# Kernel optimization log

Measured on AMD Instinct MI355X. Metric: run time of the kernel, lower is better.

Reference implementation:

```python
import jax, jax.numpy as jnp
from jax import lax
import numpy as np

D_MODEL = 1024
D_STATE = 16
D_CONV = 4
EXPAND = 2
D_INNER = EXPAND * D_MODEL          # 2048
DT_RANK = D_MODEL // 16             # 64 (mamba 'auto' dt_rank)
B, L = 1, 1024


def setup_inputs() -> dict:
    key = jax.random.key(0)
    ks = jax.random.split(key, 8)

    def nrm(k, shape, s=0.02):
        return jax.random.normal(k, shape, jnp.float32) * s

    def mamba_params(kbase):
        k = jax.random.split(kbase, 7)
        return {
            'in_w': nrm(k[0], (2 * D_INNER, D_MODEL)),            # in_proj (no bias)
            'conv_w': nrm(k[1], (D_INNER, 1, D_CONV), 0.1),       # depthwise causal conv
            'conv_b': nrm(k[2], (D_INNER,), 0.1),
            'xproj_w': nrm(k[3], (DT_RANK + 2 * D_STATE, D_INNER)),
            'dt_w': nrm(k[4], (D_INNER, DT_RANK), 0.1),
            'dt_b': nrm(k[5], (D_INNER,), 0.1),
            'Alog': jnp.log(jnp.broadcast_to(jnp.arange(1., D_STATE + 1, dtype=jnp.float32), (D_INNER, D_STATE))),
            'Dp': jnp.ones((D_INNER,), jnp.float32),
            'out_w': nrm(k[6], (D_MODEL, D_INNER)),
        }

    fw = mamba_params(ks[0])
    bw = mamba_params(ks[1])
    inp = {'x': jax.random.normal(ks[2], (B, L, D_MODEL), jnp.float32)}
    for n, p in fw.items():
        inp['fw_' + n] = p
    for n, p in bw.items():
        inp['bw_' + n] = p
    inp['proj_w'] = nrm(ks[3], (D_MODEL, 2 * D_MODEL))
    inp['proj_b'] = jnp.zeros((D_MODEL,), jnp.float32)
    inp['ln_w'] = jnp.ones((D_MODEL,), jnp.float32)
    inp['ln_b'] = jnp.zeros((D_MODEL,), jnp.float32)
    return inp


def _mamba(x, in_w, conv_w, conv_b, xproj_w, dt_w, dt_b, Alog, Dp, out_w):
    # x: [B, L, d_model]
    xz = x @ in_w.T                                    # [B, L, 2*d_inner]
    xi, z = jnp.split(xz, 2, axis=-1)
    # causal depthwise conv over time
    xc = lax.conv_general_dilated(jnp.swapaxes(xi, 1, 2), conv_w, (1,),
                                  [(D_CONV - 1, 0)], feature_group_count=D_INNER)
    u = jnp.swapaxes(jax.nn.silu(xc + conv_b[None, :, None]), 1, 2)   # [B, L, d_inner]
    x_dbl = u @ xproj_w.T                              # [B, L, dt_rank + 2*d_state]
    dt = x_dbl[..., :DT_RANK]
    Bm = x_dbl[..., DT_RANK:DT_RANK + D_STATE]
    Cm = x_dbl[..., DT_RANK + D_STATE:]
    delta = jax.nn.softplus(dt @ dt_w.T + dt_b)        # [B, L, d_inner]
    A = -jnp.exp(Alog)                                 # [d_inner, d_state]
    dA = jnp.exp(jnp.einsum('bld,dn->bldn', delta, A))
    dBu = jnp.einsum('bld,bln,bld->bldn', delta, Bm, u)

    def step(h, inputs):
        a, b, c = inputs                               # a,b: [B,D,N]; c: [B,N]
        h = a * h + b
        return h, jnp.einsum('bdn,bn->bd', h, c)

    h0 = jnp.zeros((x.shape[0], D_INNER, D_STATE), x.dtype)
    _, ys = lax.scan(step, h0, (jnp.moveaxis(dA, 1, 0), jnp.moveaxis(dBu, 1, 0), jnp.moveaxis(Cm, 1, 0)))
    y = jnp.moveaxis(ys, 0, 1) + u * Dp                # [B, L, d_inner]
    return (y * jax.nn.silu(z)) @ out_w.T              # [B, L, d_model]


def _block(x,
           fw_in_w, fw_conv_w, fw_conv_b, fw_xproj_w, fw_dt_w, fw_dt_b, fw_Alog, fw_Dp, fw_out_w,
           bw_in_w, bw_conv_w, bw_conv_b, bw_xproj_w, bw_dt_w, bw_dt_b, bw_Alog, bw_Dp, bw_out_w,
           proj_w, proj_b, ln_w, ln_b):
    out_fw = _mamba(x, fw_in_w, fw_conv_w, fw_conv_b, fw_xproj_w, fw_dt_w, fw_dt_b, fw_Alog, fw_Dp, fw_out_w) + x
    xb = jnp.flip(x, axis=1)
    out_bw = jnp.flip(_mamba(xb, bw_in_w, bw_conv_w, bw_conv_b, bw_xproj_w, bw_dt_w, bw_dt_b, bw_Alog, bw_Dp, bw_out_w) + xb, axis=1)
    out = jnp.concatenate([out_fw, out_bw], axis=-1) @ proj_w.T + proj_b
    mu = out.mean(-1, keepdims=True)
    var = out.var(-1, keepdims=True)
    return (out - mu) / jnp.sqrt(var + 1e-5) * ln_w + ln_b


def reference(x,
              fw_in_w, fw_conv_w, fw_conv_b, fw_xproj_w, fw_dt_w, fw_dt_b, fw_Alog, fw_Dp, fw_out_w,
              bw_in_w, bw_conv_w, bw_conv_b, bw_xproj_w, bw_dt_w, bw_dt_b, bw_Alog, bw_Dp, bw_out_w,
              proj_w, proj_b, ln_w, ln_b):
    return _block(x,
                  fw_in_w, fw_conv_w, fw_conv_b, fw_xproj_w, fw_dt_w, fw_dt_b, fw_Alog, fw_Dp, fw_out_w,
                  bw_in_w, bw_conv_w, bw_conv_b, bw_xproj_w, bw_dt_w, bw_dt_b, bw_Alog, bw_Dp, bw_out_w,
                  proj_w, proj_b, ln_w, ln_b)
```

## Files before the change

### kernel.cpp

```cpp
#include <hip/hip_runtime.h>

typedef __bf16 bf16;
typedef __bf16 bf16x8 __attribute__((ext_vector_type(8)));
typedef float  f32x4  __attribute__((ext_vector_type(4)));

#define L_SEQ 1024
#define DM    1024
#define DI    2048
#define DTR   64
#define DSTATE 16
#define XD    96
#define NC    32
#define CS    32

__device__ __forceinline__ float bf2f(bf16 v){ return (float)v; }
__device__ __forceinline__ bf16  f2bf(float v){ return (bf16)v; }

__device__ __forceinline__ void gl_lds16(const bf16* g, bf16* l) {
  __builtin_amdgcn_global_load_lds(
      (const __attribute__((address_space(1))) unsigned int*)g,
      (__attribute__((address_space(3))) unsigned int*)l, 16, 0, 0);
}

#define OFF_X      0L
#define OFF_INW    1048576L
#define OFF_XPROJ  9437184L
#define OFF_DTW    9830400L
#define OFF_OUTW   10092544L
#define OFF_PROJW  14286848L
#define CVT_TOTAL  16384000L

__global__ __launch_bounds__(256) void cvt_k(
    const float* __restrict__ x,
    const float* __restrict__ inw0, const float* __restrict__ inw1,
    const float* __restrict__ xp0,  const float* __restrict__ xp1,
    const float* __restrict__ dt0,  const float* __restrict__ dt1,
    const float* __restrict__ ow0,  const float* __restrict__ ow1,
    const float* __restrict__ pw,   bf16* __restrict__ wb)
{
  long i = ((long)blockIdx.x * 256 + threadIdx.x) * 8;
  if (i >= CVT_TOTAL) return;
  const float* src; long off;
  if      (i < OFF_INW)                 { src = x;    off = i - OFF_X; }
  else if (i < OFF_INW + 4194304L)      { src = inw0; off = i - OFF_INW; }
  else if (i < OFF_XPROJ)               { src = inw1; off = i - (OFF_INW + 4194304L); }
  else if (i < OFF_XPROJ + 196608L)     { src = xp0;  off = i - OFF_XPROJ; }
  else if (i < OFF_DTW)                 { src = xp1;  off = i - (OFF_XPROJ + 196608L); }
  else if (i < OFF_DTW + 131072L)       { src = dt0;  off = i - OFF_DTW; }
  else if (i < OFF_OUTW)                { src = dt1;  off = i - (OFF_DTW + 131072L); }
  else if (i < OFF_OUTW + 2097152L)     { src = ow0;  off = i - OFF_OUTW; }
  else if (i < OFF_PROJW)               { src = ow1;  off = i - (OFF_OUTW + 2097152L); }
  else                                  { src = pw;   off = i - OFF_PROJW; }
  f32x4 v0 = *(const f32x4*)(src + off);
  f32x4 v1 = *(const f32x4*)(src + off + 4);
  bf16x8 t;
  #pragma unroll
  for (int q = 0; q < 4; q++) { t[q] = (bf16)v0[q]; t[4+q] = (bf16)v1[q]; }
  *(bf16x8*)(wb + i) = t;
}

template<int BM, int BN>
__global__ __launch_bounds__(256) void gemm_bt(
    const bf16* __restrict__ A, const bf16* __restrict__ B0, const bf16* __restrict__ B1,
    void* __restrict__ Cv,
    int M, int N, int K, int lda, int ldb, int ldc,
    long aOffZ, long cOffZ,
    const float* __restrict__ bias0, const float* __restrict__ bias1,
    int flipA1, int writeBf16, int act,
    const float* __restrict__ xF, int fuseRes)
{
  constexpr int WM = BM / 2, WN = BN / 2;
  constexpr int MI = WM / 16, NJ = WN / 16;
  constexpr int ACALLS = BM / 32;
  constexpr int BCALLS = BN / 32;

  const int tid  = threadIdx.x;
  const int z    = blockIdx.z;
  const bf16*  Bp   = z ? B1 : B0;
  const float* bias = z ? bias1 : bias0;
  const int flip = z ? flipA1 : 0;
  const int bm = blockIdx.x * BM;
  const int bn = blockIdx.y * BN;

  __shared__ bf16 As[BM * 64];
  __shared__ bf16 Bs[BN * 64];

  f32x4 acc[MI][NJ];
  #pragma unroll
  for (int i=0;i<MI;i++)
    #pragma unroll
    for (int j=0;j<NJ;j++) { acc[i][j][0]=0.f; acc[i][j][1]=0.f; acc[i][j][2]=0.f; acc[i][j][3]=0.f; }

  const int wave = tid >> 6;
  const int lane = tid & 63;
  const int wm = (wave >> 1) * WM;
  const int wn = (wave & 1) * WN;
  const int fr  = lane & 15;
  const int frx = fr & 7;
  const int kqc = lane >> 4;

  const bf16* aSrc[ACALLS];
  int aOff[ACALLS];
  #pragma unroll
  for (int t = 0; t < ACALLS; t++) {
    int s = (wave * ACALLS + t) * 64 + lane;
    int r = s >> 3;
    int j = (s & 7) ^ (r & 7);
    int ar = bm + r;
    int agr = flip ? (M - 1 - ar) : ar;
    aSrc[t] = A + (long)z * aOffZ + (long)agr * lda + j * 8;
    aOff[t] = (wave * ACALLS + t) * 512;
  }
  const bf16* bSrc[BCALLS];
  int bOff[BCALLS];
  #pragma unroll
  for (int t = 0; t < BCALLS; t++) {
    int s = (wave * BCALLS + t) * 64 + lane;
    int r = s >> 3;
    int j = (s & 7) ^ (r & 7);
    int br = bn + r; if (br > N - 1) br = N - 1;
    bSrc[t] = Bp + (long)br * ldb + j * 8;
    bOff[t] = (wave * BCALLS + t) * 512;
  }

  for (int k0 = 0; k0 < K; k0 += 64) {
    #pragma unroll
    for (int t = 0; t < ACALLS; t++) gl_lds16(aSrc[t] + k0, &As[aOff[t]]);
    #pragma unroll
    for (int t = 0; t < BCALLS; t++) gl_lds16(bSrc[t] + k0, &Bs[bOff[t]]);
    __syncthreads();

    #pragma unroll
    for (int ks8 = 0; ks8 < 8; ks8 += 4) {
      bf16x8 af[MI], bfr[NJ];
      #pragma unroll
      for (int i=0;i<MI;i++) {
        int row = wm + i*16 + fr;
        af[i]  = *(const bf16x8*)&As[(row * 8 + ((ks8 + kqc) ^ frx)) * 8];
      }
      #pragma unroll
      for (int j=0;j<NJ;j++) {
        int row = wn + j*16 + fr;
        bfr[j] = *(const bf16x8*)&Bs[(row * 8 + ((ks8 + kqc) ^ frx)) * 8];
      }
      #pragma unroll
      for (int i=0;i<MI;i++)
        #pragma unroll
        for (int j=0;j<NJ;j++)
          acc[i][j] = __builtin_amdgcn_mfma_f32_16x16x32_bf16(af[i], bfr[j], acc[i][j], 0, 0, 0);
    }
    __syncthreads();
  }

  const int rr = (lane >> 4) * 4;
  const int cc = lane & 15;
  #pragma unroll
  for (int i=0;i<MI;i++) {
    #pragma unroll
    for (int j=0;j<NJ;j++) {
      int gn = bn + wn + j*16 + cc;
      if (gn >= N) continue;
      float bv = bias ? bias[gn] : 0.f;
      #pragma unroll
      for (int r=0;r<4;r++) {
        int gm = bm + wm + i*16 + rr + r;
        float v = acc[i][j][r] + bv;
        if (fuseRes) {
          long row = z ? (long)(M - 1 - gm) : (long)gm;
          float o = v + xF[row * DM + gn];
          ((bf16*)Cv)[row * (2 * DM) + (long)z * DM + gn] = f2bf(o);
        } else {
          if (act == 1) v = (v > 20.f) ? v : log1pf(__expf(v));
          long idx = (long)z * cOffZ + (long)gm * ldc + gn;
          if (writeBf16) ((bf16*)Cv)[idx] = f2bf(v);
          else           ((float*)Cv)[idx] = v;
        }
      }
    }
  }
}

__global__ __launch_bounds__(256) void conv_silu_k(
    const bf16* __restrict__ xz, const float* __restrict__ cw0, const float* __restrict__ cw1,
    const float* __restrict__ cb0, const float* __restrict__ cb1, bf16* __restrict__ u)
{
  int gid = blockIdx.x * 256 + threadIdx.x;
  int dir = gid >> 18;
  int rem = gid & ((1 << 18) - 1);
  int l = rem >> 8;
  int d0 = (rem & 255) * 8;
  const float* w = dir ? cw1 : cw0;
  const float* b = dir ? cb1 : cb0;
  const bf16* xzd = xz + (long)dir * L_SEQ * (2 * DI);
  float acc[8];
  #pragma unroll
  for (int q = 0; q < 8; q++) acc[q] = b[d0 + q];
  #pragma unroll
  for (int j = 0; j < 4; j++) {
    int ll = l - 3 + j;
    if (ll < 0) continue;
    bf16x8 xv = *(const bf16x8*)(xzd + (long)ll * (2 * DI) + d0);
    #pragma unroll
    for (int q = 0; q < 8; q++) acc[q] += w[(d0 + q) * 4 + j] * bf2f(xv[q]);
  }
  bf16x8 o;
  #pragma unroll
  for (int q = 0; q < 8; q++) {
    float s = acc[q] / (1.f + __expf(-acc[q]));
    o[q] = f2bf(s);
  }
  *(bf16x8*)(u + (long)dir * L_SEQ * DI + (long)l * DI + d0) = o;
}

__global__ __launch_bounds__(256) void scan_p1(
    const bf16* __restrict__ xz, const bf16* __restrict__ u, const bf16* __restrict__ xdbl,
    const float* __restrict__ Alog0, const float* __restrict__ Alog1,
    bf16* __restrict__ hout, float* __restrict__ sumd)
{
  const int tid = threadIdx.x;
  const int c   = blockIdx.y;
  const int dir = blockIdx.z;
  const int d   = blockIdx.x * 256 + tid;
  const float* Alog = dir ? Alog1 : Alog0;
  const bf16* dl = xz + (long)dir * L_SEQ * (2 * DI);
  const bf16* ud = u  + (long)dir * L_SEQ * DI;
  const bf16* xd = xdbl + (long)dir * L_SEQ * XD;
  const int l0 = c * CS;

  __shared__ float lb[CS][16];
  {
    int i = tid * 2;
    int ll = i >> 4, n = i & 15;
    const bf16* p = xd + (long)(l0 + ll) * XD + DTR + n;
    lb[ll][n]     = bf2f(p[0]);
    lb[ll][n + 1] = bf2f(p[1]);
  }
  __syncthreads();

  float An[16], h[16];
  #pragma unroll
  for (int n = 0; n < 16; n++) { An[n] = -__expf(Alog[d * 16 + n]); h[n] = 0.f; }
  float sd = 0.f;

  #pragma unroll 4
  for (int ll = 0; ll < CS; ll++) {
    int l = l0 + ll;
    float dlt = bf2f(dl[(long)l * (2 * DI) + d]);
    float uu  = bf2f(ud[(long)l * DI + d]);
    sd += dlt;
    float du = dlt * uu;
    #pragma unroll
    for (int n = 0; n < 16; n++) {
      float a = __expf(dlt * An[n]);
      h[n] = h[n] * a + du * lb[ll][n];
    }
  }

  bf16* hp = hout + (((long)dir * NC + c) * DI + d) * 16;
  bf16x8 o0, o1;
  #pragma unroll
  for (int n = 0; n < 8; n++) { o0[n] = f2bf(h[n]); o1[n] = f2bf(h[8 + n]); }
  *(bf16x8*)hp = o0;
  *(bf16x8*)(hp + 8) = o1;
  sumd[((long)dir * NC + c) * DI + d] = sd;
}

__global__ __launch_bounds__(256) void scan_p23(
    const bf16* xz, const bf16* u, const bf16* __restrict__ xdbl,
    const float* __restrict__ Alog0, const float* __restrict__ Alog1,
    const float* __restrict__ Dp0, const float* __restrict__ Dp1,
    const bf16* __restrict__ hout, const float* __restrict__ sumd, bf16* g)
{
  const int tid = threadIdx.x;
  const int c   = blockIdx.y;
  const int dir = blockIdx.z;
  const int d   = blockIdx.x * 256 + tid;
  const float* Alog = dir ? Alog1 : Alog0;
  const float* Dp   = dir ? Dp1 : Dp0;
  const bf16* row0 = xz + (long)dir * L_SEQ * (2 * DI);
  const bf16* ud   = u  + (long)dir * L_SEQ * DI;
  const bf16* xd   = xdbl + (long)dir * L_SEQ * XD;
  bf16* gd = g + (long)dir * L_SEQ * DI;
  const int l0 = c * CS;

  __shared__ float lb[CS][16];
  __shared__ float lc[CS][16];
  {
    int i = tid * 4;
    int ll = i >> 5, j = i & 31;
    const bf16* p = xd + (long)(l0 + ll) * XD + DTR + j;
    #pragma unroll
    for (int q = 0; q < 4; q++) {
      int jj = j + q;
      float v = bf2f(p[q]);
      if (jj < 16) lb[ll][jj] = v; else lc[ll][jj - 16] = v;
    }
  }
  __syncthreads();

  float An[16], h[16];
  #pragma unroll
  for (int n = 0; n < 16; n++) {
    An[n] = -__expf(Alog[d * 16 + n]);
    h[n] = 0.f;
  }

  for (int cp = 0; cp < c; cp++) {
    long base = ((long)dir * NC + cp) * DI + d;
    float sd = sumd[base];
    const bf16* hp = hout + base * 16;
    bf16x8 s0 = *(const bf16x8*)hp;
    bf16x8 s1 = *(const bf16x8*)(hp + 8);
    #pragma unroll
    for (int n = 0; n < 16; n++) {
      float P = __expf(An[n] * sd);
      float S = bf2f(n < 8 ? s0[n & 7] : s1[n & 7]);
      h[n] = P * h[n] + S;
    }
  }

  const float Dpv = Dp[d];
  #pragma unroll 4
  for (int ll = 0; ll < CS; ll++) {
    int l = l0 + ll;
    float dlt = bf2f(row0[(long)l * (2 * DI) + d]);
    float zv  = bf2f(row0[(long)l * (2 * DI) + DI + d]);
    float uu  = bf2f(ud[(long)l * DI + d]);
    float du = dlt * uu;
    float y = 0.f;
    #pragma unroll
    for (int n = 0; n < 16; n++) {
      float a = __expf(dlt * An[n]);
      h[n] = h[n] * a + du * lb[ll][n];
      y += h[n] * lc[ll][n];
    }
    y += uu * Dpv;
    float sz = zv / (1.f + __expf(-zv));
    gd[(long)l * DI + d] = f2bf(y * sz);
  }
}

__global__ __launch_bounds__(256) void ln_k(
    const float* __restrict__ fin, const float* __restrict__ pb,
    const float* __restrict__ lnw, const float* __restrict__ lnb, float* __restrict__ out)
{
  int row = blockIdx.x;
  int tid = threadIdx.x;
  float v[4]; float s1 = 0.f, s2 = 0.f;
  #pragma unroll
  for (int j = 0; j < 4; j++) {
    int c = tid + j * 256;
    v[j] = fin[(long)row * DM + c] + pb[c];
    s1 += v[j]; s2 += v[j] * v[j];
  }
  #pragma unroll
  for (int off = 32; off; off >>= 1) { s1 += __shfl_down(s1, off); s2 += __shfl_down(s2, off); }
  __shared__ float red[8];
  int wave = tid >> 6, lane = tid & 63;
  if (lane == 0) { red[wave] = s1; red[4 + wave] = s2; }
  __syncthreads();
  float t1 = red[0] + red[1] + red[2] + red[3];
  float t2 = red[4] + red[5] + red[6] + red[7];
  float mu = t1 / DM;
  float var = t2 / DM - mu * mu;
  float inv = rsqrtf(var + 1e-5f);
  #pragma unroll
  for (int j = 0; j < 4; j++) {
    int c = tid + j * 256;
    out[(long)row * DM + c] = (v[j] - mu) * inv * lnw[c] + lnb[c];
  }
}

extern "C" void kernel_launch(void* const* d_in, const int* in_sizes, int n_in,
                              void* d_out, int out_size, void* d_ws, size_t ws_size,
                              hipStream_t stream)
{
  const float* x         = (const float*)d_in[0];
  const float* fw_conv_w = (const float*)d_in[2];
  const float* fw_conv_b = (const float*)d_in[3];
  const float* fw_dt_b   = (const float*)d_in[6];
  const float* fw_Alog   = (const float*)d_in[7];
  const float* fw_Dp     = (const float*)d_in[8];
  const float* bw_conv_w = (const float*)d_in[11];
  const float* bw_conv_b = (const float*)d_in[12];
  const float* bw_dt_b   = (const float*)d_in[15];
  const float* bw_Alog   = (const float*)d_in[16];
  const float* bw_Dp     = (const float*)d_in[17];
  const float* proj_b    = (const float*)d_in[20];
  const float* ln_w      = (const float*)d_in[21];
  const float* ln_b      = (const float*)d_in[22];

  char* ws = (char*)d_ws;
  const size_t MB = 1024 * 1024;
  bf16*  xz    = (bf16*)(ws + 0);
  bf16*  u     = (bf16*)(ws + 16 * MB);
  bf16*  xdbl  = (bf16*)(ws + 24 * MB);
  float* sumd  = (float*)(ws + 25 * MB);
  bf16*  hout  = (bf16*)(ws + 26 * MB);
  bf16*  wb    = (bf16*)(ws + 30 * MB);
  bf16*  g     = u;
  bf16*  delta = xz;
  bf16*  fused = (bf16*)(ws + 0);
  float* fin   = (float*)(ws + 4 * MB);

  bf16* xb     = wb + OFF_X;
  bf16* inw    = wb + OFF_INW;
  bf16* xprojw = wb + OFF_XPROJ;
  bf16* dtw    = wb + OFF_DTW;
  bf16* outw   = wb + OFF_OUTW;
  bf16* projw  = wb + OFF_PROJW;

  dim3 blk(256);

  cvt_k<<<(CVT_TOTAL / 8 + 255) / 256, blk, 0, stream>>>(
      x, (const float*)d_in[1], (const float*)d_in[10],
      (const float*)d_in[4], (const float*)d_in[13],
      (const float*)d_in[5], (const float*)d_in[14],
      (const float*)d_in[9], (const float*)d_in[18],
      (const float*)d_in[19], wb);

  gemm_bt<64,128><<<dim3(16, 32, 2), blk, 0, stream>>>(
      xb, inw, inw + 4194304L, (void*)xz, 1024, 4096, 1024, 1024, 1024, 4096,
      0L, (long)1024 * 4096, nullptr, nullptr, 1, 1, 0, nullptr, 0);

  conv_silu_k<<<2048, blk, 0, stream>>>(xz, fw_conv_w, bw_conv_w, fw_conv_b, bw_conv_b, u);

  gemm_bt<32,64><<<dim3(32, 2, 2), blk, 0, stream>>>(
      u, xprojw, xprojw + 196608L, (void*)xdbl, 1024, 96, 2048, 2048, 2048, 96,
      (long)1024 * 2048, (long)1024 * 96, nullptr, nullptr, 0, 1, 0, nullptr, 0);

  gemm_bt<64,128><<<dim3(16, 16, 2), blk, 0, stream>>>(
      xdbl, dtw, dtw + 131072L, (void*)delta, 1024, 2048, 64, 96, 64, 4096,
      (long)1024 * 96, (long)1024 * 4096, fw_dt_b, bw_dt_b, 0, 1, 1, nullptr, 0);

  scan_p1<<<dim3(8, NC, 2), blk, 0, stream>>>(xz, u, xdbl, fw_Alog, bw_Alog, hout, sumd);
  scan_p23<<<dim3(8, NC, 2), blk, 0, stream>>>(xz, u, xdbl, fw_Alog, bw_Alog,
                                               fw_Dp, bw_Dp, hout, sumd, g);

  gemm_bt<32,64><<<dim3(32, 16, 2), blk, 0, stream>>>(
      g, outw, outw + 2097152L, (void*)fused, 1024, 1024, 2048, 2048, 2048, 1024,
      (long)1024 * 2048, 0L, nullptr, nullptr, 0, 1, 0, x, 1);

  gemm_bt<32,64><<<dim3(32, 16, 1), blk, 0, stream>>>(
      fused, projw, projw, (void*)fin, 1024, 1024, 2048, 2048, 2048, 1024,
      0L, 0L, nullptr, nullptr, 0, 0, 0, nullptr, 0);

  ln_k<<<1024, blk, 0, stream>>>(fin, proj_b, ln_w, ln_b, (float*)d_out);
}
```

Baseline: 365.6 us.

## Split chunked scan into three passes with a separate carry-propagation kernel

Replaces the per-chunk quadratic re-accumulation of prior chunk states in scan_p23 with a dedicated scan_p2 kernel that computes exclusive prefix carries once per (dir, d, n), so scan_p3 just loads its starting state. It also doubles the number of chunks while halving chunk length to raise parallelism, and preloads the per-timestep delta, u and z values into registers before the recurrence. The extra kernel launch and larger hout workspace, which moves the weight buffer offset, are the cost. Register pressure from the fully unrolled arrays may limit occupancy.

New measurement: 336.4 us. -8.0%, faster.

```diff
diff --git a/kernel.cpp b/kernel.cpp
--- a/kernel.cpp
+++ b/kernel.cpp
@@ -10,8 +10,8 @@
 #define DTR   64
 #define DSTATE 16
 #define XD    96
-#define NC    32
-#define CS    32
+#define NC    64
+#define CS    16
 
 __device__ __forceinline__ float bf2f(bf16 v){ return (float)v; }
 __device__ __forceinline__ bf16  f2bf(float v){ return (bf16)v; }
@@ -229,11 +229,15 @@
 
   __shared__ float lb[CS][16];
   {
-    int i = tid * 2;
-    int ll = i >> 4, n = i & 15;
-    const bf16* p = xd + (long)(l0 + ll) * XD + DTR + n;
-    lb[ll][n]     = bf2f(p[0]);
-    lb[ll][n + 1] = bf2f(p[1]);
+    int ll = tid >> 4, n = tid & 15;
+    lb[ll][n] = bf2f(xd[(long)(l0 + ll) * XD + DTR + n]);
+  }
+
+  float dl_r[CS], uu_r[CS];
+  #pragma unroll
+  for (int s = 0; s < CS; s++) {
+    dl_r[s] = bf2f(dl[(long)(l0 + s) * (2 * DI) + d]);
+    uu_r[s] = bf2f(ud[(long)(l0 + s) * DI + d]);
   }
   __syncthreads();
 
@@ -242,13 +246,11 @@
   for (int n = 0; n < 16; n++) { An[n] = -__expf(Alog[d * 16 + n]); h[n] = 0.f; }
   float sd = 0.f;
 
-  #pragma unroll 4
+  #pragma unroll
   for (int ll = 0; ll < CS; ll++) {
-    int l = l0 + ll;
-    float dlt = bf2f(dl[(long)l * (2 * DI) + d]);
-    float uu  = bf2f(ud[(long)l * DI + d]);
+    float dlt = dl_r[ll];
     sd += dlt;
-    float du = dlt * uu;
+    float du = dlt * uu_r[ll];
     #pragma unroll
     for (int n = 0; n < 16; n++) {
       float a = __expf(dlt * An[n]);
@@ -265,11 +267,33 @@
   sumd[((long)dir * NC + c) * DI + d] = sd;
 }
 
-__global__ __launch_bounds__(256) void scan_p23(
+__global__ __launch_bounds__(256) void scan_p2(
+    const float* __restrict__ Alog0, const float* __restrict__ Alog1,
+    bf16* hout, const float* __restrict__ sumd)
+{
+  int g = blockIdx.x * 256 + threadIdx.x;
+  int dir = g >> 15;
+  int rem = g & 32767;
+  int d = rem >> 4;
+  int n = rem & 15;
+  const float* Alog = dir ? Alog1 : Alog0;
+  float An = -__expf(Alog[d * 16 + n]);
+  float hs = 0.f;
+  #pragma unroll 4
+  for (int c = 0; c < NC; c++) {
+    long base = ((long)dir * NC + c) * DI + d;
+    float tmp = bf2f(hout[base * 16 + n]);
+    float P = __expf(An * sumd[base]);
+    hout[base * 16 + n] = f2bf(hs);
+    hs = P * hs + tmp;
+  }
+}
+
+__global__ __launch_bounds__(256) void scan_p3(
     const bf16* xz, const bf16* u, const bf16* __restrict__ xdbl,
     const float* __restrict__ Alog0, const float* __restrict__ Alog1,
     const float* __restrict__ Dp0, const float* __restrict__ Dp1,
-    const bf16* __restrict__ hout, const float* __restrict__ sumd, bf16* g)
+    const bf16* __restrict__ hout, bf16* g)
 {
   const int tid = threadIdx.x;
   const int c   = blockIdx.y;
@@ -286,47 +310,38 @@
   __shared__ float lb[CS][16];
   __shared__ float lc[CS][16];
   {
-    int i = tid * 4;
+    int i = tid * 2;
     int ll = i >> 5, j = i & 31;
     const bf16* p = xd + (long)(l0 + ll) * XD + DTR + j;
-    #pragma unroll
-    for (int q = 0; q < 4; q++) {
-      int jj = j + q;
-      float v = bf2f(p[q]);
-      if (jj < 16) lb[ll][jj] = v; else lc[ll][jj - 16] = v;
-    }
-  }
+    float v0 = bf2f(p[0]), v1 = bf2f(p[1]);
+    if (j < 16) { lb[ll][j] = v0; lb[ll][j + 1] = v1; }
+    else        { lc[ll][j - 16] = v0; lc[ll][j - 15] = v1; }
+  }
+
+  float dl_r[CS], uu_r[CS], zv_r[CS];
+  #pragma unroll
+  for (int s = 0; s < CS; s++) {
+    dl_r[s] = bf2f(row0[(long)(l0 + s) * (2 * DI) + d]);
+    zv_r[s] = bf2f(row0[(long)(l0 + s) * (2 * DI) + DI + d]);
+    uu_r[s] = bf2f(ud[(long)(l0 + s) * DI + d]);
+  }
+  const bf16* hp = hout + (((long)dir * NC + c) * DI + d) * 16;
+  bf16x8 h0 = *(const bf16x8*)hp;
+  bf16x8 h1 = *(const bf16x8*)(hp + 8);
   __syncthreads();
 
   float An[16], h[16];
   #pragma unroll
   for (int n = 0; n < 16; n++) {
     An[n] = -__expf(Alog[d * 16 + n]);
-    h[n] = 0.f;
-  }
-
-  for (int cp = 0; cp < c; cp++) {
-    long base = ((long)dir * NC + cp) * DI + d;
-    float sd = sumd[base];
-    const bf16* hp = hout + base * 16;
-    bf16x8 s0 = *(const bf16x8*)hp;
-    bf16x8 s1 = *(const bf16x8*)(hp + 8);
-    #pragma unroll
-    for (int n = 0; n < 16; n++) {
-      float P = __expf(An[n] * sd);
-      float S = bf2f(n < 8 ? s0[n & 7] : s1[n & 7]);
-      h[n] = P * h[n] + S;
-    }
-  }
-
+    h[n] = bf2f(n < 8 ? h0[n & 7] : h1[n & 7]);
+  }
   const float Dpv = Dp[d];
-  #pragma unroll 4
+
+  #pragma unroll
   for (int ll = 0; ll < CS; ll++) {
-    int l = l0 + ll;
-    float dlt = bf2f(row0[(long)l * (2 * DI) + d]);
-    float zv  = bf2f(row0[(long)l * (2 * DI) + DI + d]);
-    float uu  = bf2f(ud[(long)l * DI + d]);
-    float du = dlt * uu;
+    float dlt = dl_r[ll];
+    float du = dlt * uu_r[ll];
     float y = 0.f;
     #pragma unroll
     for (int n = 0; n < 16; n++) {
@@ -334,9 +349,10 @@
       h[n] = h[n] * a + du * lb[ll][n];
       y += h[n] * lc[ll][n];
     }
-    y += uu * Dpv;
+    y += uu_r[ll] * Dpv;
+    float zv = zv_r[ll];
     float sz = zv / (1.f + __expf(-zv));
-    gd[(long)l * DI + d] = f2bf(y * sz);
+    gd[(long)(l0 + ll) * DI + d] = f2bf(y * sz);
   }
 }
 
@@ -397,7 +413,7 @@
   bf16*  xdbl  = (bf16*)(ws + 24 * MB);
   float* sumd  = (float*)(ws + 25 * MB);
   bf16*  hout  = (bf16*)(ws + 26 * MB);
-  bf16*  wb    = (bf16*)(ws + 30 * MB);
+  bf16*  wb    = (bf16*)(ws + 34 * MB);
   bf16*  g     = u;
   bf16*  delta = xz;
   bf16*  fused = (bf16*)(ws + 0);
@@ -434,8 +450,9 @@
       (long)1024 * 96, (long)1024 * 4096, fw_dt_b, bw_dt_b, 0, 1, 1, nullptr, 0);
 
   scan_p1<<<dim3(8, NC, 2), blk, 0, stream>>>(xz, u, xdbl, fw_Alog, bw_Alog, hout, sumd);
-  scan_p23<<<dim3(8, NC, 2), blk, 0, stream>>>(xz, u, xdbl, fw_Alog, bw_Alog,
-                                               fw_Dp, bw_Dp, hout, sumd, g);
+  scan_p2<<<dim3(256), blk, 0, stream>>>(fw_Alog, bw_Alog, hout, sumd);
+  scan_p3<<<dim3(8, NC, 2), blk, 0, stream>>>(xz, u, xdbl, fw_Alog, bw_Alog,
+                                              fw_Dp, bw_Dp, hout, g);
 
   gemm_bt<32,64><<<dim3(32, 16, 2), blk, 0, stream>>>(
       g, outw, outw + 2097152L, (void*)fused, 1024, 1024, 2048, 2048, 2048, 1024,
```
